# Optimization experiments

Measured on AMD Instinct MI355X. Metric: run time of the kernel, lower is better.

## Reference

```python
import jax, jax.numpy as jnp
import numpy as np

NB_OBJECTS = 3
DIM_BODY = 10
DIM_OBJECT = 15
DIM_ACT = 4
DIM_NODE = 128
D_PHI_IN = DIM_ACT + DIM_BODY + DIM_OBJECT + DIM_NODE  # 157
HID = 256
D_PHI_OUT = 3 * D_PHI_IN  # 471
D_RHO_OUT = 1
BATCH = 65536


def _linear_init(key, fan_in, fan_out):
    # torch nn.Linear default: U(-1/sqrt(fan_in), 1/sqrt(fan_in))
    bound = 1.0 / np.sqrt(fan_in)
    k1, k2 = jax.random.split(key)
    W = jax.random.uniform(k1, (fan_in, fan_out), minval=-bound, maxval=bound, dtype=jnp.float32)
    b = jax.random.uniform(k2, (fan_out,), minval=-bound, maxval=bound, dtype=jnp.float32)
    return W, b


def setup_inputs() -> dict:
    key = jax.random.key(0)
    ks = jax.random.split(key, 11)
    obs = jax.random.normal(ks[0], (BATCH, DIM_BODY + NB_OBJECTS * DIM_OBJECT), dtype=jnp.float32)
    act = jax.random.normal(ks[1], (BATCH, DIM_ACT), dtype=jnp.float32)
    nodes = jax.random.normal(ks[2], (NB_OBJECTS, BATCH, DIM_NODE), dtype=jnp.float32)
    phi1_w1, phi1_b1 = _linear_init(ks[3], D_PHI_IN, HID)
    phi1_w2, phi1_b2 = _linear_init(ks[4], HID, D_PHI_OUT)
    phi2_w1, phi2_b1 = _linear_init(ks[5], D_PHI_IN, HID)
    phi2_w2, phi2_b2 = _linear_init(ks[6], HID, D_PHI_OUT)
    rho1_w1, rho1_b1 = _linear_init(ks[7], D_PHI_OUT, HID)
    rho1_w2, rho1_b2 = _linear_init(ks[8], HID, D_RHO_OUT)
    rho2_w1, rho2_b1 = _linear_init(ks[9], D_PHI_OUT, HID)
    rho2_w2, rho2_b2 = _linear_init(ks[10], HID, D_RHO_OUT)
    return {
        "obs": obs, "act": act, "nodes": nodes,
        "phi1_w1": phi1_w1, "phi1_b1": phi1_b1, "phi1_w2": phi1_w2, "phi1_b2": phi1_b2,
        "phi2_w1": phi2_w1, "phi2_b1": phi2_b1, "phi2_w2": phi2_w2, "phi2_b2": phi2_b2,
        "rho1_w1": rho1_w1, "rho1_b1": rho1_b1, "rho1_w2": rho1_w2, "rho1_b2": rho1_b2,
        "rho2_w1": rho2_w1, "rho2_b1": rho2_b1, "rho2_w2": rho2_w2, "rho2_b2": rho2_b2,
    }


def reference(obs, act, nodes,
              phi1_w1, phi1_b1, phi1_w2, phi1_b2,
              phi2_w1, phi2_b1, phi2_w2, phi2_b2,
              rho1_w1, rho1_b1, rho1_w2, rho1_b2,
              rho2_w1, rho2_b1, rho2_w2, rho2_b2):
    B = obs.shape[0]
    obs_body = obs[:, :DIM_BODY]                                   # [B, 10]
    # per-object slices -> [nb_objects, B, dim_object]
    obs_obj = obs[:, DIM_BODY:].reshape(B, NB_OBJECTS, DIM_OBJECT).transpose(1, 0, 2)
    shared = jnp.concatenate([act, obs_body], axis=-1)             # [B, 14]
    shared = jnp.broadcast_to(shared[None], (NB_OBJECTS, B, shared.shape[-1]))
    inp_phi = jnp.concatenate([shared, obs_obj, nodes], axis=-1)   # [3, B, 157]

    def mlp2(x, w1, b1, w2, b2):
        h = jax.nn.relu(x @ w1 + b1)
        return jax.nn.relu(h @ w2 + b2)

    # DeepSet: per-entity phi then sum over entities
    out1 = mlp2(inp_phi, phi1_w1, phi1_b1, phi1_w2, phi1_b2).sum(axis=0)  # [B, 471]
    out2 = mlp2(inp_phi, phi2_w1, phi2_b1, phi2_w2, phi2_b2).sum(axis=0)
    q1 = jax.nn.relu(out1 @ rho1_w1 + rho1_b1) @ rho1_w2 + rho1_b2        # [B, 1]
    q2 = jax.nn.relu(out2 @ rho2_w1 + rho2_b1) @ rho2_w2 + rho2_b2
    return (q1, q2)
```

## Files before the change

### kernel.cpp

```cpp
#include <hip/hip_runtime.h>
#include <hip/hip_fp16.h>

typedef _Float16 half8 __attribute__((ext_vector_type(8)));
typedef float f32x4 __attribute__((ext_vector_type(4)));

#define BATCH 65536
#define M1 196608
#define K1 160

#define GLL16(g, l) __builtin_amdgcn_global_load_lds( \
    (const __attribute__((address_space(1))) unsigned int*)(const void*)(g), \
    (__attribute__((address_space(3))) unsigned int*)(void*)(l), 16, 0, 0)

__global__ void prep_kernel(const float* __restrict__ p1w1, const float* __restrict__ p2w1,
                            const float* __restrict__ p1w2, const float* __restrict__ p2w2,
                            const float* __restrict__ r1w1, const float* __restrict__ r2w1,
                            const float* __restrict__ p1b1, const float* __restrict__ p2b1,
                            const float* __restrict__ p1b2, const float* __restrict__ p2b2,
                            const float* __restrict__ rb1a, const float* __restrict__ rb1b,
                            _Float16* __restrict__ W1t, _Float16* __restrict__ W2t,
                            _Float16* __restrict__ R1t, float* __restrict__ b1cat,
                            float* __restrict__ b2cat, float* __restrict__ rbias) {
    int e = blockIdx.x * 256 + threadIdx.x;
    if (e < 81920) {
        int n = e / 160, c = e % 160;
        int k = (c < 128) ? (29 + c) : (c - 128);
        float v = 0.f;
        if (c < 157) v = (n < 256) ? p1w1[k * 256 + n] : p2w1[k * 256 + (n - 256)];
        W1t[e] = (_Float16)v;
        return;
    }
    e -= 81920;
    if (e < 262144) {
        int net = e >> 17, rr = e & 131071;
        int n = rr >> 8, k = rr & 255;
        const float* w = net ? p2w2 : p1w2;
        W2t[(size_t)net * 131072 + rr] = (n < 471) ? (_Float16)w[k * 471 + n] : (_Float16)0.f;
        return;
    }
    e -= 262144;
    if (e < 262144) {
        int net = e >> 17, rr = e & 131071;
        int n = rr >> 9, k = rr & 511;
        const float* w = net ? r2w1 : r1w1;
        R1t[(size_t)net * 131072 + rr] = (k < 471) ? (_Float16)w[k * 256 + n] : (_Float16)0.f;
        return;
    }
    e -= 262144;
    if (e < 512) { b1cat[e] = (e < 256) ? p1b1[e] : p2b1[e - 256]; return; }
    e -= 512;
    if (e < 1024) {
        int net = e >> 9, n = e & 511;
        b2cat[e] = (n < 471) ? (net ? p2b2 : p1b2)[n] : 0.f;
        return;
    }
    e -= 1024;
    if (e < 512) {
        int net = e >> 8, n = e & 255;
        rbias[e] = (net ? rb1b : rb1a)[n];
    }
}

__global__ void build_x(const float* __restrict__ obs, const float* __restrict__ act,
                        const float* __restrict__ nodes, _Float16* __restrict__ Xh) {
    long idx = (long)blockIdx.x * 256 + threadIdx.x;
    int ch = (int)(idx % 20);
    long r = idx / 20;
    int o = (int)(r >> 16), b = (int)(r & 65535);
    half8 v;
    if (ch < 16) {
        const float* s = nodes + r * 128 + ch * 8;
#pragma unroll
        for (int j = 0; j < 8; ++j) v[j] = (_Float16)s[j];
    } else {
#pragma unroll
        for (int j = 0; j < 8; ++j) {
            int lc = ch * 8 + j - 128;
            float f = 0.f;
            if (lc < 4)       f = act[b * 4 + lc];
            else if (lc < 14) f = obs[b * 55 + (lc - 4)];
            else if (lc < 29) f = obs[b * 55 + 10 + o * 15 + (lc - 14)];
            v[j] = (_Float16)f;
        }
    }
    *(half8*)(Xh + r * K1 + ch * 8) = v;
}


__global__ __launch_bounds__(256) void gemm1(const _Float16* __restrict__ Xh,
                                             const _Float16* __restrict__ W1t,
                                             const float* __restrict__ b1cat,
                                             _Float16* __restrict__ H) {
    __shared__ _Float16 As[2][4096];
    __shared__ _Float16 Bs[2][4096];
    const int tid = threadIdx.x;
    int bid = blockIdx.x;
    int w = (bid & 7) * 768 + (bid >> 3);
    const int m0 = (w >> 2) * 128, n0 = (w & 3) * 128;
    const _Float16* Ab = Xh + (long)m0 * K1;
    const _Float16* Bb = W1t + (long)n0 * K1;
    const int wid = tid >> 6, lane = tid & 63;
    const int lm = lane & 15, lq = lane >> 4;
    const int wr = (wid >> 1) * 64, wc = (wid & 1) * 64;

    auto stage = [&](int s, int buf) {
        int ko = s * 32;
#pragma unroll
        for (int t = 0; t < 2; ++t) {
            int c = t * 256 + tid, row = c >> 2, chk = c & 3;
            int q = chk ^ ((row >> 1) & 3);
            GLL16(Ab + (long)row * K1 + ko + q * 8, &As[buf][0] + t * 2048 + wid * 512);
            GLL16(Bb + (long)row * K1 + ko + q * 8, &Bs[buf][0] + t * 2048 + wid * 512);
        }
    };

    stage(0, 0);
    __syncthreads();

    const int cc = (lq ^ ((lm >> 1) & 3)) * 8;
    f32x4 acc[4][4] = {};
    int cur = 0;
#pragma unroll
    for (int r = 0; r < 5; ++r) {
        if (r < 4) stage(r + 1, cur ^ 1);
        const _Float16* ab = &As[cur][0];
        const _Float16* bb = &Bs[cur][0];
        half8 a[4], b[4];
#pragma unroll
        for (int i = 0; i < 4; ++i) a[i] = *(const half8*)(ab + (wr + i * 16 + lm) * 32 + cc);
#pragma unroll
        for (int j = 0; j < 4; ++j) b[j] = *(const half8*)(bb + (wc + j * 16 + lm) * 32 + cc);
#pragma unroll
        for (int i = 0; i < 4; ++i)
#pragma unroll
            for (int j = 0; j < 4; ++j)
                acc[i][j] = __builtin_amdgcn_mfma_f32_16x16x32_f16(a[i], b[j], acc[i][j], 0, 0, 0);
        __syncthreads();
        cur ^= 1;
    }
#pragma unroll
    for (int j = 0; j < 4; ++j) {
        int n = n0 + wc + j * 16 + lm;
        int net = n >> 8, ncol = n & 255;
        float bi = b1cat[n];
        _Float16* hp = H + (long)net * ((long)M1 * 256) + ncol;
#pragma unroll
        for (int i = 0; i < 4; ++i) {
            int mrow = m0 + wr + i * 16 + lq * 4;
#pragma unroll
            for (int rg = 0; rg < 4; ++rg) {
                float v = acc[i][j][rg] + bi;
                v = v > 0.f ? v : 0.f;
                hp[(long)(mrow + rg) * 256] = (_Float16)v;
            }
        }
    }
}

__global__ __launch_bounds__(256) void gemm_sum(const _Float16* __restrict__ H,
                                                const _Float16* __restrict__ W2t,
                                                const float* __restrict__ b2cat,
                                                _Float16* __restrict__ Osum) {
    __shared__ _Float16 As[2][8192];
    __shared__ _Float16 Bs[2][8192];
    const int tid = threadIdx.x;
    int bid = blockIdx.x;
    int w = (bid & 7) * 512 + (bid >> 3);
    const int n0 = (w & 3) * 128, net = (w >> 2) & 1, b0 = (w >> 3) * 128;
    const _Float16* Ab = H + (long)net * ((long)M1 * 256) + (long)b0 * 256;
    const _Float16* Bb = W2t + (long)net * 131072 + (long)n0 * 256;
    const int wid = tid >> 6, lane = tid & 63;
    const int lm = lane & 15, lq = lane >> 4;
    const int wr = (wid >> 1) * 64, wc = (wid & 1) * 64;

    float bi[4];
#pragma unroll
    for (int j = 0; j < 4; ++j) bi[j] = b2cat[net * 512 + n0 + wc + j * 16 + lm];

    auto stage = [&](int s, int buf) {
        int obj = s >> 2, ko = (s & 3) * 64;
        const _Float16* Ao = Ab + (long)obj * BATCH * 256;
#pragma unroll
        for (int t = 0; t < 4; ++t) {
            int c = t * 256 + tid, row = c >> 3, chk = c & 7;
            int q = chk ^ (row & 7);
            GLL16(Ao + (long)row * 256 + ko + q * 8, &As[buf][0] + t * 2048 + wid * 512);
            GLL16(Bb + (long)row * 256 + ko + q * 8, &Bs[buf][0] + t * 2048 + wid * 512);
        }
    };

    stage(0, 0);
    __syncthreads();

    const int xv = lm & 7;
    f32x4 acc[4][4] = {};
    f32x4 sum[4][4] = {};
    int cur = 0;
    for (int r = 0; r < 12; ++r) {
        if (r < 11) stage(r + 1, cur ^ 1);
        const _Float16* ab = &As[cur][0];
        const _Float16* bb = &Bs[cur][0];
#pragma unroll
        for (int ks = 0; ks < 2; ++ks) {
            const int off = ((ks * 4 + lq) ^ xv) * 8;
            half8 a[4], b[4];
#pragma unroll
            for (int i = 0; i < 4; ++i) a[i] = *(const half8*)(ab + (wr + i * 16 + lm) * 64 + off);
#pragma unroll
            for (int j = 0; j < 4; ++j) b[j] = *(const half8*)(bb + (wc + j * 16 + lm) * 64 + off);
#pragma unroll
            for (int i = 0; i < 4; ++i)
#pragma unroll
                for (int j = 0; j < 4; ++j)
                    acc[i][j] = __builtin_amdgcn_mfma_f32_16x16x32_f16(a[i], b[j], acc[i][j], 0, 0, 0);
        }
        if ((r & 3) == 3) {
#pragma unroll
            for (int i = 0; i < 4; ++i)
#pragma unroll
                for (int j = 0; j < 4; ++j) {
#pragma unroll
                    for (int rg = 0; rg < 4; ++rg) {
                        float v = acc[i][j][rg] + bi[j];
                        sum[i][j][rg] += (v > 0.f ? v : 0.f);
                    }
                    acc[i][j] = f32x4{0.f, 0.f, 0.f, 0.f};
                }
        }
        __syncthreads();
        cur ^= 1;
    }
    _Float16* op = Osum + (long)net * ((long)BATCH * 512);
#pragma unroll
    for (int j = 0; j < 4; ++j) {
        int n = n0 + wc + j * 16 + lm;
#pragma unroll
        for (int i = 0; i < 4; ++i) {
            int mrow = b0 + wr + i * 16 + lq * 4;
#pragma unroll
            for (int rg = 0; rg < 4; ++rg)
                op[(long)(mrow + rg) * 512 + n] = (_Float16)sum[i][j][rg];
        }
    }
}

__global__ __launch_bounds__(512) void gemm3q(const _Float16* __restrict__ Osum,
                                              const _Float16* __restrict__ R1t,
                                              const float* __restrict__ rbias,
                                              const float* __restrict__ r1w2,
                                              const float* __restrict__ r2w2,
                                              const float* __restrict__ r1b2,
                                              const float* __restrict__ r2b2,
                                              float* __restrict__ out) {
    __shared__ _Float16 As[2][8192];
    __shared__ _Float16 Bs[2][16384];
    __shared__ float qlds[128];
    const int tid = threadIdx.x;
    int bid = blockIdx.x;
    int w = (bid & 7) * 128 + (bid >> 3);
    const int net = w & 1, b0 = (w >> 1) * 128;
    if (tid < 128) qlds[tid] = 0.f;
    const _Float16* Ab = Osum + (long)net * ((long)BATCH * 512) + (long)b0 * 512;
    const _Float16* Bb = R1t + (long)net * 131072;
    const int wid = tid >> 6, lane = tid & 63;
    const int lm = lane & 15, lq = lane >> 4;
    const int wr = (wid >> 2) * 64, wc = (wid & 3) * 64;
    const int xv = lm & 7;
    const int srow = tid >> 3, schk = tid & 7;

    auto stage = [&](int s, int buf) {
        int ko = s * 64;
#pragma unroll
        for (int g = 0; g < 2; ++g) {
            int row = srow + g * 64, q = schk ^ (row & 7);
            GLL16(Ab + (long)row * 512 + ko + q * 8, &As[buf][0] + g * 4096 + wid * 512);
        }
#pragma unroll
        for (int g = 0; g < 4; ++g) {
            int row = srow + g * 64, q = schk ^ (row & 7);
            GLL16(Bb + (long)row * 512 + ko + q * 8, &Bs[buf][0] + g * 4096 + wid * 512);
        }
    };

    stage(0, 0);
    __syncthreads();

    f32x4 acc[4][4] = {};
    int cur = 0;
    for (int r = 0; r < 8; ++r) {
        if (r < 7) stage(r + 1, cur ^ 1);
        const _Float16* ab = &As[cur][0];
        const _Float16* bb = &Bs[cur][0];
#pragma unroll
        for (int ks = 0; ks < 2; ++ks) {
            const int off = ((ks * 4 + lq) ^ xv) * 8;
            half8 a[4], b[4];
#pragma unroll
            for (int i = 0; i < 4; ++i) a[i] = *(const half8*)(ab + (wr + i * 16 + lm) * 64 + off);
#pragma unroll
            for (int j = 0; j < 4; ++j) b[j] = *(const half8*)(bb + (wc + j * 16 + lm) * 64 + off);
#pragma unroll
            for (int i = 0; i < 4; ++i)
#pragma unroll
                for (int j = 0; j < 4; ++j)
                    acc[i][j] = __builtin_amdgcn_mfma_f32_16x16x32_f16(a[i], b[j], acc[i][j], 0, 0, 0);
        }
        __syncthreads();
        cur ^= 1;
    }
    const float* w2 = net ? r2w2 : r1w2;
    const float* rb = rbias + net * 256;
    float w2v[4], bv[4];
#pragma unroll
    for (int j = 0; j < 4; ++j) {
        int col = wc + j * 16 + lm;
        w2v[j] = w2[col];
        bv[j] = rb[col];
    }
    f32x4 qp[4] = {};
#pragma unroll
    for (int i = 0; i < 4; ++i)
#pragma unroll
        for (int j = 0; j < 4; ++j)
#pragma unroll
            for (int rg = 0; rg < 4; ++rg) {
                float v = acc[i][j][rg] + bv[j];
                v = v > 0.f ? v : 0.f;
                qp[i][rg] += v * w2v[j];
            }
#pragma unroll
    for (int d = 1; d < 16; d <<= 1)
#pragma unroll
        for (int i = 0; i < 4; ++i)
#pragma unroll
            for (int rg = 0; rg < 4; ++rg)
                qp[i][rg] += __shfl_xor(qp[i][rg], d, 64);
    if ((lane & 15) == 0) {
#pragma unroll
        for (int i = 0; i < 4; ++i)
#pragma unroll
            for (int rg = 0; rg < 4; ++rg)
                atomicAdd(&qlds[wr + i * 16 + lq * 4 + rg], qp[i][rg]);
    }
    __syncthreads();
    if (tid < 128)
        out[(long)net * BATCH + b0 + tid] = qlds[tid] + (net ? r2b2[0] : r1b2[0]);
}

extern "C" void kernel_launch(void* const* d_in, const int* in_sizes, int n_in,
                              void* d_out, int out_size, void* d_ws, size_t ws_size,
                              hipStream_t stream) {
    const float* obs  = (const float*)d_in[0];
    const float* act  = (const float*)d_in[1];
    const float* nodes= (const float*)d_in[2];
    const float* p1w1 = (const float*)d_in[3];  const float* p1b1 = (const float*)d_in[4];
    const float* p1w2 = (const float*)d_in[5];  const float* p1b2 = (const float*)d_in[6];
    const float* p2w1 = (const float*)d_in[7];  const float* p2b1 = (const float*)d_in[8];
    const float* p2w2 = (const float*)d_in[9];  const float* p2b2 = (const float*)d_in[10];
    const float* r1w1 = (const float*)d_in[11]; const float* r1b1 = (const float*)d_in[12];
    const float* r1w2 = (const float*)d_in[13]; const float* r1b2 = (const float*)d_in[14];
    const float* r2w1 = (const float*)d_in[15]; const float* r2b1 = (const float*)d_in[16];
    const float* r2w2 = (const float*)d_in[17]; const float* r2b2 = (const float*)d_in[18];

    const size_t oW1t  = 0;
    const size_t oW2t  = 163840;
    const size_t oR1t  = 688128;
    const size_t oB1   = 1212416;
    const size_t oB2   = 1214464;
    const size_t oRB   = 1218560;
    const size_t oXO   = 1220608;
    const size_t oH    = 135438336;
    const size_t need  = 336764928;
    if (ws_size < need) return;

    char* ws = (char*)d_ws;
    _Float16* W1t  = (_Float16*)(ws + oW1t);
    _Float16* W2t  = (_Float16*)(ws + oW2t);
    _Float16* R1t  = (_Float16*)(ws + oR1t);
    float*    b1cat= (float*)(ws + oB1);
    float*    b2cat= (float*)(ws + oB2);
    float*    rbias= (float*)(ws + oRB);
    _Float16* Xh   = (_Float16*)(ws + oXO);
    _Float16* Osum = (_Float16*)(ws + oXO);
    _Float16* H    = (_Float16*)(ws + oH);
    float* out = (float*)d_out;

    prep_kernel<<<2376, 256, 0, stream>>>(p1w1, p2w1, p1w2, p2w2, r1w1, r2w1,
                                          p1b1, p2b1, p1b2, p2b2, r1b1, r2b1,
                                          W1t, W2t, R1t, b1cat, b2cat, rbias);
    build_x<<<15360, 256, 0, stream>>>(obs, act, nodes, Xh);
    gemm1<<<6144, 256, 0, stream>>>(Xh, W1t, b1cat, H);
    gemm_sum<<<4096, 256, 0, stream>>>(H, W2t, b2cat, Osum);
    gemm3q<<<1024, 512, 0, stream>>>(Osum, R1t, rbias, r1w2, r2w2, r1b2, r2b2, out);
}
```

Measured before the change: 342.5 us.

## Replace LDS-tiled phi second-layer GEMM with register-resident weights and direct global loads

Rewrites the second phi GEMM plus object-sum kernel to drop LDS staging entirely. Each wave now keeps its 32-column slice of W2 in registers for the whole K=256 and streams H rows straight from global memory into MFMA operands, using a 64x128 tile and twice as many blocks. This removes LDS traffic and the barriers between stages. In exchange, every wave reloads the same A rows from global/L2 with no sharing across waves, and register use goes up.

```diff
diff --git a/kernel.cpp b/kernel.cpp
--- a/kernel.cpp
+++ b/kernel.cpp
@@ -86,7 +86,6 @@
     *(half8*)(Xh + r * K1 + ch * 8) = v;
 }
 
-
 __global__ __launch_bounds__(256) void gemm1(const _Float16* __restrict__ Xh,
                                              const _Float16* __restrict__ W1t,
                                              const float* __restrict__ b1cat,
@@ -157,86 +156,66 @@
     }
 }
 
-__global__ __launch_bounds__(256) void gemm_sum(const _Float16* __restrict__ H,
-                                                const _Float16* __restrict__ W2t,
-                                                const float* __restrict__ b2cat,
-                                                _Float16* __restrict__ Osum) {
-    __shared__ _Float16 As[2][8192];
-    __shared__ _Float16 Bs[2][8192];
+__global__ __launch_bounds__(256) void gemm_sum_flat(const _Float16* __restrict__ H,
+                                                     const _Float16* __restrict__ W2t,
+                                                     const float* __restrict__ b2cat,
+                                                     _Float16* __restrict__ Osum) {
     const int tid = threadIdx.x;
     int bid = blockIdx.x;
-    int w = (bid & 7) * 512 + (bid >> 3);
-    const int n0 = (w & 3) * 128, net = (w >> 2) & 1, b0 = (w >> 3) * 128;
-    const _Float16* Ab = H + (long)net * ((long)M1 * 256) + (long)b0 * 256;
-    const _Float16* Bb = W2t + (long)net * 131072 + (long)n0 * 256;
+    int w = (bid & 7) * 1024 + (bid >> 3);
+    const int nq = w & 3, net = (w >> 2) & 1, mt = w >> 3;
     const int wid = tid >> 6, lane = tid & 63;
     const int lm = lane & 15, lq = lane >> 4;
-    const int wr = (wid >> 1) * 64, wc = (wid & 1) * 64;
-
-    float bi[4];
-#pragma unroll
-    for (int j = 0; j < 4; ++j) bi[j] = b2cat[net * 512 + n0 + wc + j * 16 + lm];
-
-    auto stage = [&](int s, int buf) {
-        int obj = s >> 2, ko = (s & 3) * 64;
-        const _Float16* Ao = Ab + (long)obj * BATCH * 256;
-#pragma unroll
-        for (int t = 0; t < 4; ++t) {
-            int c = t * 256 + tid, row = c >> 3, chk = c & 7;
-            int q = chk ^ (row & 7);
-            GLL16(Ao + (long)row * 256 + ko + q * 8, &As[buf][0] + t * 2048 + wid * 512);
-            GLL16(Bb + (long)row * 256 + ko + q * 8, &Bs[buf][0] + t * 2048 + wid * 512);
-        }
-    };
-
-    stage(0, 0);
-    __syncthreads();
-
-    const int xv = lm & 7;
-    f32x4 acc[4][4] = {};
-    f32x4 sum[4][4] = {};
-    int cur = 0;
-    for (int r = 0; r < 12; ++r) {
-        if (r < 11) stage(r + 1, cur ^ 1);
-        const _Float16* ab = &As[cur][0];
-        const _Float16* bb = &Bs[cur][0];
-#pragma unroll
-        for (int ks = 0; ks < 2; ++ks) {
-            const int off = ((ks * 4 + lq) ^ xv) * 8;
-            half8 a[4], b[4];
-#pragma unroll
-            for (int i = 0; i < 4; ++i) a[i] = *(const half8*)(ab + (wr + i * 16 + lm) * 64 + off);
-#pragma unroll
-            for (int j = 0; j < 4; ++j) b[j] = *(const half8*)(bb + (wc + j * 16 + lm) * 64 + off);
+    const int wc = wid * 32, n0 = nq * 128;
+
+    const _Float16* Wb = W2t + (long)net * 131072;
+    half8 breg[2][8];
+#pragma unroll
+    for (int j = 0; j < 2; ++j) {
+        const _Float16* wp = Wb + (long)(n0 + wc + j * 16 + lm) * 256 + lq * 8;
+#pragma unroll
+        for (int s = 0; s < 8; ++s)
+            breg[j][s] = *(const half8*)(wp + s * 32);
+    }
+    float bi[2];
+#pragma unroll
+    for (int j = 0; j < 2; ++j) bi[j] = b2cat[net * 512 + n0 + wc + j * 16 + lm];
+
+    f32x4 sum[4][2] = {};
+    const long rowbase = (long)net * M1 + (long)mt * 64;
+#pragma unroll
+    for (int obj = 0; obj < 3; ++obj) {
+        const _Float16* Ab = H + (rowbase + (long)obj * BATCH + lm) * 256 + lq * 8;
+        f32x4 acc[4][2] = {};
+#pragma unroll
+        for (int s = 0; s < 8; ++s) {
+            half8 a[4];
 #pragma unroll
             for (int i = 0; i < 4; ++i)
-#pragma unroll
-                for (int j = 0; j < 4; ++j)
-                    acc[i][j] = __builtin_amdgcn_mfma_f32_16x16x32_f16(a[i], b[j], acc[i][j], 0, 0, 0);
-        }
-        if ((r & 3) == 3) {
+                a[i] = *(const half8*)(Ab + (long)i * 4096 + s * 32);
 #pragma unroll
             for (int i = 0; i < 4; ++i)
 #pragma unroll
-                for (int j = 0; j < 4; ++j) {
-#pragma unroll
-                    for (int rg = 0; rg < 4; ++rg) {
-                        float v = acc[i][j][rg] + bi[j];
-                        sum[i][j][rg] += (v > 0.f ? v : 0.f);
-                    }
-                    acc[i][j] = f32x4{0.f, 0.f, 0.f, 0.f};
+                for (int j = 0; j < 2; ++j)
+                    acc[i][j] = __builtin_amdgcn_mfma_f32_16x16x32_f16(a[i], breg[j][s], acc[i][j], 0, 0, 0);
+        }
+#pragma unroll
+        for (int i = 0; i < 4; ++i)
+#pragma unroll
+            for (int j = 0; j < 2; ++j)
+#pragma unroll
+                for (int rg = 0; rg < 4; ++rg) {
+                    float v = acc[i][j][rg] + bi[j];
+                    sum[i][j][rg] += (v > 0.f ? v : 0.f);
                 }
-        }
-        __syncthreads();
-        cur ^= 1;
     }
     _Float16* op = Osum + (long)net * ((long)BATCH * 512);
 #pragma unroll
-    for (int j = 0; j < 4; ++j) {
+    for (int j = 0; j < 2; ++j) {
         int n = n0 + wc + j * 16 + lm;
 #pragma unroll
         for (int i = 0; i < 4; ++i) {
-            int mrow = b0 + wr + i * 16 + lq * 4;
+            int mrow = mt * 64 + i * 16 + lq * 4;
 #pragma unroll
             for (int rg = 0; rg < 4; ++rg)
                 op[(long)(mrow + rg) * 512 + n] = (_Float16)sum[i][j][rg];
@@ -390,6 +369,6 @@
                                           W1t, W2t, R1t, b1cat, b2cat, rbias);
     build_x<<<15360, 256, 0, stream>>>(obs, act, nodes, Xh);
     gemm1<<<6144, 256, 0, stream>>>(Xh, W1t, b1cat, H);
-    gemm_sum<<<4096, 256, 0, stream>>>(H, W2t, b2cat, Osum);
+    gemm_sum_flat<<<8192, 256, 0, stream>>>(H, W2t, b2cat, Osum);
     gemm3q<<<1024, 512, 0, stream>>>(Osum, R1t, rbias, r1w2, r2w2, r1b2, r2b2, out);
 }
```

New measurement: 574.6 us. 1.68x slower.
